# Kernel tuning notes

Measured on AMD Instinct MI355X. Metric: run time of the kernel, lower is better.

Reference implementation:

```python
import jax, jax.numpy as jnp
import numpy as np
from jax import lax

NSAMPLE = 16
NEG_SLOPE = 0.1


def leaky(x):
    return jnp.where(x >= 0, x, NEG_SLOPE * x)


def setup_inputs() -> dict:
    key = jax.random.key(0)
    ks = jax.random.split(key, 8)
    B, N1, N2, D = 4, 4096, 4096, 64
    C_in, C_mid, C_out = D + D + 3, 128, 128  # 131 -> 128 -> 128
    xyz1 = jax.random.normal(ks[0], (B, 3, N1), jnp.float32)
    xyz2 = jax.random.normal(ks[1], (B, 3, N2), jnp.float32)
    points1 = jax.random.normal(ks[2], (B, D, N1), jnp.float32)
    points2 = jax.random.normal(ks[3], (B, D, N2), jnp.float32)
    W1 = jax.random.normal(ks[4], (C_mid, C_in), jnp.float32) * 0.05
    b1 = jnp.zeros((C_mid,), jnp.float32)
    W2 = jax.random.normal(ks[5], (C_out, C_mid), jnp.float32) * 0.05
    b2 = jnp.zeros((C_out,), jnp.float32)
    return {"xyz1": xyz1, "xyz2": xyz2, "points1": points1, "points2": points2,
            "W1": W1, "b1": b1, "W2": W2, "b2": b2}


def reference(xyz1, xyz2, points1, points2, W1, b1, W2, b2):
    B, _, N1 = xyz1.shape
    x1 = jnp.transpose(xyz1, (0, 2, 1))      # [B,N1,3]
    x2 = jnp.transpose(xyz2, (0, 2, 1))      # [B,N2,3]
    p1 = jnp.transpose(points1, (0, 2, 1))   # [B,N1,D1]
    p2 = jnp.transpose(points2, (0, 2, 1))   # [B,N2,D2]

    # knn_point: k smallest squared distances from each x1 point into x2
    d2 = (jnp.sum(x1 * x1, -1)[:, :, None]
          + jnp.sum(x2 * x2, -1)[:, None, :]
          - 2.0 * jnp.einsum('bnc,bmc->bnm', x1, x2))  # [B,N1,N2]
    _, knn_idx = lax.top_k(-d2, NSAMPLE)     # [B,N1,K]

    bidx = jnp.arange(B)[:, None, None]
    neighbor_xyz = x2[bidx, knn_idx]         # [B,N1,K,3]
    direction_xyz = neighbor_xyz - x1[:, :, None, :]
    gp2 = p2[bidx, knn_idx]                  # [B,N1,K,D2]
    gp1 = jnp.broadcast_to(p1[:, :, None, :], (B, N1, NSAMPLE, p1.shape[-1]))
    feat = jnp.concatenate([gp1, gp2, direction_xyz], axis=-1)  # [B,N1,K,131]

    h = leaky(jnp.einsum('oc,bnkc->bnko', W1, feat) + b1)
    h = leaky(jnp.einsum('oc,bnkc->bnko', W2, h) + b2)           # [B,N1,K,C_out]

    dist = jnp.maximum(jnp.linalg.norm(direction_xyz, axis=3), 1e-10)  # [B,N1,K]
    inv = 1.0 / dist
    weights = inv / jnp.sum(inv, axis=2, keepdims=True)          # [B,N1,K]

    cost = jnp.einsum('bnk,bnko->bon', weights, h)               # [B,C_out,N1]
    return cost
```

## Files before the change

### kernel.cpp

```cpp
#include <hip/hip_runtime.h>

typedef unsigned short u16;
typedef unsigned int u32;
typedef unsigned long long u64;
typedef __bf16 bf16x8 __attribute__((ext_vector_type(8)));
typedef float f32x4 __attribute__((ext_vector_type(4)));

#define MFMA16(a, b, c) __builtin_amdgcn_mfma_f32_16x16x32_bf16(a, b, c, 0, 0, 0)

static __device__ __forceinline__ u16 f2bf(float f) {
  union { float f; u32 u; } v; v.f = f;
  u32 u = v.u;
  u32 r = (u + 0x7FFFu + ((u >> 16) & 1u)) >> 16;
  return (u16)r;
}

static __device__ __forceinline__ bf16x8 ld16(const u16* p) {
  return __builtin_bit_cast(bf16x8, *(const uint4*)p);
}

static __device__ __forceinline__ u64 u64min(u64 a, u64 b) { return a < b ? a : b; }

static __device__ __forceinline__ u64 bitonic64(u64 v, int lane) {
#pragma unroll
  for (int k = 2; k <= 64; k <<= 1) {
#pragma unroll
    for (int j = k >> 1; j > 0; j >>= 1) {
      u64 o = __shfl_xor(v, j, 64);
      bool up = ((lane & k) == 0);
      bool lower = ((lane & j) == 0);
      u64 mn = v < o ? v : o;
      u64 mx = v < o ? o : v;
      v = (lower == up) ? mn : mx;
    }
  }
  return v;
}

static __device__ __forceinline__ void bitonic64_2(u64& a, u64& b, int lane) {
#pragma unroll
  for (int k = 2; k <= 64; k <<= 1) {
#pragma unroll
    for (int j = k >> 1; j > 0; j >>= 1) {
      u64 oa = __shfl_xor(a, j, 64);
      u64 ob = __shfl_xor(b, j, 64);
      bool up = ((lane & k) == 0);
      bool lower = ((lane & j) == 0);
      bool sel = (lower == up);
      u64 mna = a < oa ? a : oa, mxa = a < oa ? oa : a;
      u64 mnb = b < ob ? b : ob, mxb = b < ob ? ob : b;
      a = sel ? mna : mxa;
      b = sel ? mnb : mxb;
    }
  }
}

static __device__ __forceinline__ void bitonic32_2(u64& a, u64& b, int lane) {
#pragma unroll
  for (int k = 2; k <= 32; k <<= 1) {
#pragma unroll
    for (int j = k >> 1; j > 0; j >>= 1) {
      u64 oa = __shfl_xor(a, j, 64);
      u64 ob = __shfl_xor(b, j, 64);
      bool up = ((lane & k) == 0);
      bool lower = ((lane & j) == 0);
      bool sel = (lower == up);
      u64 mna = a < oa ? a : oa, mxa = a < oa ? oa : a;
      u64 mnb = b < ob ? b : ob, mxb = b < ob ? ob : b;
      a = sel ? mna : mxa;
      b = sel ? mnb : mxb;
    }
  }
}

static __device__ __forceinline__ u32 fkey(float f) {
  u32 bb = __float_as_uint(f);
  u32 sgn = (u32)((int)bb >> 31);
  return bb ^ (sgn | 0x80000000u);
}

static __device__ __forceinline__ float ikey(u32 k) {
  u32 bb = (k & 0x80000000u) ? (k ^ 0x80000000u) : ~k;
  return __uint_as_float(bb);
}

static __device__ __forceinline__ float d2of(float x, float y, float z, float s1,
                                             f32x4 c) {
  float dt = __builtin_fmaf(z, c[2], __builtin_fmaf(y, c[1], __fmul_rn(x, c[0])));
  return __fsub_rn(__fadd_rn(s1, c[3]), __fmul_rn(2.0f, dt));
}

static __device__ __forceinline__ f32x4 candOf(const float* X2, int m) {
  float cx = X2[m], cy = X2[4096 + m], cz = X2[8192 + m];
  float cs = __fadd_rn(__fadd_rn(__fmul_rn(cx, cx), __fmul_rn(cy, cy)),
                       __fmul_rn(cz, cz));
  f32x4 c = {cx, cy, cz, cs};
  return c;
}

__global__ __launch_bounds__(256, 7) void knn_prep(
    const float* __restrict__ xyz1, const float* __restrict__ xyz2,
    const float* __restrict__ points1, const float* __restrict__ points2,
    const float* __restrict__ W1, const float* __restrict__ W2,
    u16* __restrict__ p1t, u16* __restrict__ p2t,
    u16* __restrict__ W1b, u16* __restrict__ W2b,
    int* __restrict__ knn) {
  __shared__ __align__(16) char LB[8448];
  u16* tile = (u16*)LB;
  u64 (*surv)[2][64] = (u64(*)[2][64])LB;
  const int t = threadIdx.x;
  const int lane = t & 63;
  const int w = t >> 6;
  const int g = blockIdx.x;

  if (g < 144) {
    int i = g * 256 + t;
    if (i < 128 * 160) {
      int r = i / 160, c = i - r * 160;
      W1b[i] = (c < 131) ? f2bf(W1[r * 131 + c]) : (u16)0;
    } else {
      int u = i - 128 * 160;
      W2b[u] = f2bf(W2[u]);
    }
  }

  {
    const bool doT = (g < 512);
    const float* src = (g < 256) ? points1 : points2;
    u16* dst = (g < 256) ? p1t : p2t;
    const int gb = g & 255;
    const int tb = gb >> 6;
    const int n0 = (gb & 63) << 6;
    const float* sp = src + ((size_t)tb << 18);
    if (doT) {
#pragma unroll
      for (int i = 0; i < 16; i++) {
        int d = (i << 2) + (t >> 6);
        int n = t & 63;
        tile[n * 66 + d] = f2bf(sp[((size_t)d << 12) + n0 + n]);
      }
    }
    __syncthreads();
    if (doT) {
      u16* dp = dst + ((size_t)(tb * 4096 + n0) << 6);
#pragma unroll
      for (int i = 0; i < 8; i++) {
        int n = (i << 3) + (t >> 5);
        int dp2 = t & 31;
        *(u32*)(dp + n * 64 + (dp2 << 1)) =
            *(const u32*)(tile + n * 66 + (dp2 << 1));
      }
    }
  }
  __syncthreads();

  const int b = g >> 9;
  const int rbase = (g & 511) << 3;
  const float* X1 = xyz1 + b * 12288;
  const float* X2 = xyz2 + b * 12288;
  {
    const int n0 = rbase + (w << 1);
    const int n1 = n0 + 1;
    const int row0 = b * 4096 + n0;
    const int row1 = row0 + 1;
    const float x0 = X1[n0], y0 = X1[4096 + n0], z0 = X1[8192 + n0];
    const float x1 = X1[n1], y1 = X1[4096 + n1], z1 = X1[8192 + n1];
    const float s10 = __fadd_rn(__fadd_rn(__fmul_rn(x0, x0), __fmul_rn(y0, y0)),
                                __fmul_rn(z0, z0));
    const float s11 = __fadd_rn(__fadd_rn(__fmul_rn(x1, x1), __fmul_rn(y1, y1)),
                                __fmul_rn(z1, z1));

    float fm0 = 3e38f, fm1 = 3e38f;
#pragma unroll 4
    for (int j = 0; j < 64; j++) {
      f32x4 c = candOf(X2, (j << 6) + lane);
      fm0 = fminf(fm0, d2of(x0, y0, z0, s10, c));
      fm1 = fminf(fm1, d2of(x1, y1, z1, s11, c));
    }

    const u32 k0 = fkey(fm0), k1 = fkey(fm1);
    u32 lo0 = 0u, hi0 = 0xFFFFFFFFu, lo1 = 0u, hi1 = 0xFFFFFFFFu;
#pragma unroll
    for (int it = 0; it < 32; it++) {
      u32 md0 = lo0 + ((hi0 - lo0) >> 1);
      u32 md1 = lo1 + ((hi1 - lo1) >> 1);
      bool ge0 = __popcll(__ballot(k0 <= md0)) >= 16;
      bool ge1 = __popcll(__ballot(k1 <= md1)) >= 16;
      hi0 = ge0 ? md0 : hi0;  lo0 = ge0 ? lo0 : md0 + 1;
      hi1 = ge1 ? md1 : hi1;  lo1 = ge1 ? lo1 : md1 + 1;
    }
    const float tau0 = ikey(hi0);
    const float tau1 = ikey(hi1);

    u32 base0 = 0, base1 = 0;
#pragma unroll 4
    for (int j = 0; j < 64; j++) {
      const int m = (j << 6) + lane;
      f32x4 c = candOf(X2, m);
      float d0 = d2of(x0, y0, z0, s10, c);
      float d1 = d2of(x1, y1, z1, s11, c);
      bool p0 = d0 <= tau0;
      bool p1 = d1 <= tau1;
      u64 mk0 = __ballot(p0);
      u64 mk1 = __ballot(p1);
      if (mk0) {
        if (p0) {
          u32 pre = __builtin_amdgcn_mbcnt_lo((u32)mk0, 0u);
          pre = __builtin_amdgcn_mbcnt_hi((u32)(mk0 >> 32), pre);
          u32 slot = base0 + pre;
          if (slot < 64u) surv[w][0][slot] = ((u64)fkey(d0) << 32) | (u32)m;
        }
        base0 += (u32)__popcll(mk0);
      }
      if (mk1) {
        if (p1) {
          u32 pre = __builtin_amdgcn_mbcnt_lo((u32)mk1, 0u);
          pre = __builtin_amdgcn_mbcnt_hi((u32)(mk1 >> 32), pre);
          u32 slot = base1 + pre;
          if (slot < 64u) surv[w][1][slot] = ((u64)fkey(d1) << 32) | (u32)m;
        }
        base1 += (u32)__popcll(mk1);
      }
    }
    const u32 S0 = base0, S1 = base1;

    const u32 Smax = max(S0, S1);
    if (Smax <= 32) {
      u64 v0 = (lane < (int)S0) ? surv[w][0][lane] : ~0ull;
      u64 v1 = (lane < (int)S1) ? surv[w][1][lane] : ~0ull;
      bitonic32_2(v0, v1, lane);
      if (lane < 16) {
        knn[row0 * 16 + lane] = (int)(v0 & 0xFFFFFFFFull);
        knn[row1 * 16 + lane] = (int)(v1 & 0xFFFFFFFFull);
      }
    } else if (Smax <= 64) {
      u64 v0 = (lane < (int)S0) ? surv[w][0][lane] : ~0ull;
      u64 v1 = (lane < (int)S1) ? surv[w][1][lane] : ~0ull;
      bitonic64_2(v0, v1, lane);
      if (lane < 16) {
        knn[row0 * 16 + lane] = (int)(v0 & 0xFFFFFFFFull);
        knn[row1 * 16 + lane] = (int)(v1 & 0xFFFFFFFFull);
      }
    } else {
#pragma unroll 1
      for (int p = 0; p < 2; p++) {
        const u32 S = p ? S1 : S0;
        const int row = p ? row1 : row0;
        const float xx = p ? x1 : x0, yy = p ? y1 : y0, zz = p ? z1 : z0;
        const float ss = p ? s11 : s10;
        if (S <= 64) {
          u64 v = (lane < (int)S) ? surv[w][p][lane] : ~0ull;
          v = bitonic64(v, lane);
          if (lane < 16) knn[row * 16 + lane] = (int)(v & 0xFFFFFFFFull);
        } else {
          u64 prev = 0;
          for (int rr = 0; rr < 16; rr++) {
            u64 lm = ~0ull;
#pragma unroll 4
            for (int j = 0; j < 64; j++) {
              const int m = (j << 6) + lane;
              f32x4 c = candOf(X2, m);
              float d = d2of(xx, yy, zz, ss, c);
              u64 k64 = ((u64)fkey(d) << 32) | (u32)m;
              if (k64 > prev && k64 < lm) lm = k64;
            }
            u64 gm = lm;
#pragma unroll
            for (int off = 32; off; off >>= 1)
              gm = u64min(gm, __shfl_xor(gm, off, 64));
            if (lane == 0) knn[row * 16 + rr] = (int)(gm & 0xFFFFFFFFull);
            prev = gm;
          }
        }
      }
    }
  }
}

__global__ __launch_bounds__(256, 3) void mlp_kernel(
    const float* __restrict__ xyz1, const float* __restrict__ xyz2,
    const u16* __restrict__ p1t, const u16* __restrict__ p2t,
    const int* __restrict__ knn,
    const u16* __restrict__ W1b, const float* __restrict__ b1,
    const u16* __restrict__ W2b, const float* __restrict__ b2,
    float* __restrict__ out) {
  __shared__ __align__(16) u16 F[128 * 168];
  __shared__ __align__(16) float winv[128];
  __shared__ __align__(16) float wnorm[128];
  __shared__ __align__(16) float outbuf[128 * 12];
  const int t = threadIdx.x;
  const int g = blockIdx.x;
  const int b = g >> 9;
  const int rbase = (g & 511) << 3;

  {
    const int m = t >> 1, half = t & 1;
    const int n1 = rbase + (m >> 4);
    const uint4* s1p = (const uint4*)(p1t + ((size_t)(b * 4096 + n1) << 6)) + half * 4;
    uint4* d1p = (uint4*)(F + m * 168) + half * 4;
    d1p[0] = s1p[0]; d1p[1] = s1p[1]; d1p[2] = s1p[2]; d1p[3] = s1p[3];
    const int idx = knn[(((size_t)(b * 4096 + n1)) << 4) + (m & 15)];
    const uint4* s2p = (const uint4*)(p2t + ((size_t)(b * 4096 + idx) << 6)) + half * 4;
    uint4* d2p = (uint4*)(F + m * 168 + 64) + half * 4;
    d2p[0] = s2p[0]; d2p[1] = s2p[1]; d2p[2] = s2p[2]; d2p[3] = s2p[3];
  }
  if (t < 128) {
    const int m = t;
    const int n1 = rbase + (m >> 4);
    const int idx = knn[(((size_t)(b * 4096 + n1)) << 4) + (m & 15)];
    const float* X1 = xyz1 + b * 12288;
    const float* X2 = xyz2 + b * 12288;
    float dx = X2[idx] - X1[n1];
    float dy = X2[4096 + idx] - X1[4096 + n1];
    float dz = X2[8192 + idx] - X1[8192 + n1];
    u32 u0 = (u32)f2bf(dx) | ((u32)f2bf(dy) << 16);
    u32 u1 = (u32)f2bf(dz);
    uint4 pk = make_uint4(u0, u1, 0u, 0u);
    *(uint4*)(F + m * 168 + 128) = pk;
    float d = sqrtf(dx * dx + dy * dy + dz * dz);
    winv[m] = 1.0f / fmaxf(d, 1e-10f);
  } else {
    const int m = t - 128;
    uint4 zz = make_uint4(0u, 0u, 0u, 0u);
    uint4* zp = (uint4*)(F + m * 168 + 136);
    zp[0] = zz; zp[1] = zz; zp[2] = zz; zp[3] = zz;
  }
  __syncthreads();

  if (t < 128) {
    const int r = t >> 4;
    float s = 0.f;
#pragma unroll
    for (int k = 0; k < 16; k++) s += winv[(r << 4) + k];
    wnorm[t] = winv[t] / s;
  }

  const int lane = t & 63;
  const int wid = t >> 6;
  const int l15 = lane & 15;
  const int quad = lane >> 4;
  const int koff = quad << 3;
  const int nbase = wid << 5;

  f32x4 acc[8][2];
  const f32x4 z4 = {0.f, 0.f, 0.f, 0.f};
#pragma unroll
  for (int i = 0; i < 8; i++)
#pragma unroll
    for (int j = 0; j < 2; j++) acc[i][j] = z4;

#pragma unroll
  for (int s = 0; s < 5; s++) {
    bf16x8 bf0 = ld16(W1b + (nbase + l15) * 160 + s * 32 + koff);
    bf16x8 bf1 = ld16(W1b + (nbase + 16 + l15) * 160 + s * 32 + koff);
#pragma unroll
    for (int mt = 0; mt < 8; mt++) {
      bf16x8 a = ld16(F + (mt * 16 + l15) * 168 + s * 32 + koff);
      acc[mt][0] = MFMA16(a, bf0, acc[mt][0]);
      acc[mt][1] = MFMA16(a, bf1, acc[mt][1]);
    }
  }
  __syncthreads();

  {
    const float bv0 = b1[nbase + l15];
    const float bv1 = b1[nbase + 16 + l15];
#pragma unroll
    for (int mt = 0; mt < 8; mt++) {
      u16* hrow = F + (mt * 16 + quad * 4) * 168;
#pragma unroll
      for (int r = 0; r < 4; r++) {
        float zv0 = acc[mt][0][r] + bv0;
        zv0 = (zv0 >= 0.f) ? zv0 : 0.1f * zv0;
        hrow[r * 168 + nbase + l15] = f2bf(zv0);
        float zv1 = acc[mt][1][r] + bv1;
        zv1 = (zv1 >= 0.f) ? zv1 : 0.1f * zv1;
        hrow[r * 168 + nbase + 16 + l15] = f2bf(zv1);
      }
    }
  }
  __syncthreads();

  f32x4 acc2[8][2];
#pragma unroll
  for (int i = 0; i < 8; i++)
#pragma unroll
    for (int j = 0; j < 2; j++) acc2[i][j] = z4;

#pragma unroll
  for (int s = 0; s < 4; s++) {
    bf16x8 bf0 = ld16(W2b + (nbase + l15) * 128 + s * 32 + koff);
    bf16x8 bf1 = ld16(W2b + (nbase + 16 + l15) * 128 + s * 32 + koff);
#pragma unroll
    for (int mt = 0; mt < 8; mt++) {
      bf16x8 a = ld16(F + (mt * 16 + l15) * 168 + s * 32 + koff);
      acc2[mt][0] = MFMA16(a, bf0, acc2[mt][0]);
      acc2[mt][1] = MFMA16(a, bf1, acc2[mt][1]);
    }
  }

  {
    const float bv0 = b2[nbase + l15];
    const float bv1 = b2[nbase + 16 + l15];
#pragma unroll
    for (int mt = 0; mt < 8; mt++) {
      const f32x4 w4 = *(const f32x4*)&wnorm[(mt << 4) + (quad << 2)];
      float p0 = 0.f, p1 = 0.f;
#pragma unroll
      for (int r = 0; r < 4; r++) {
        float zv0 = acc2[mt][0][r] + bv0;
        zv0 = (zv0 >= 0.f) ? zv0 : 0.1f * zv0;
        p0 += zv0 * w4[r];
        float zv1 = acc2[mt][1][r] + bv1;
        zv1 = (zv1 >= 0.f) ? zv1 : 0.1f * zv1;
        p1 += zv1 * w4[r];
      }
      p0 += __shfl_xor(p0, 16); p0 += __shfl_xor(p0, 32);
      p1 += __shfl_xor(p1, 16); p1 += __shfl_xor(p1, 32);
      if (quad == 0) {
        outbuf[(nbase + l15) * 12 + mt] = p0;
        outbuf[(nbase + 16 + l15) * 12 + mt] = p1;
      }
    }
  }
  __syncthreads();
  {
    const int ch = t >> 1, half = t & 1;
    f32x4 v = *(const f32x4*)&outbuf[ch * 12 + (half << 2)];
    float* op = out + (((size_t)(b * 128 + ch)) << 12) + rbase + (half << 2);
    *(f32x4*)op = v;
  }
}

extern "C" void kernel_launch(void* const* d_in, const int* in_sizes, int n_in,
                              void* d_out, int out_size, void* d_ws, size_t ws_size,
                              hipStream_t stream) {
  const float* xyz1 = (const float*)d_in[0];
  const float* xyz2 = (const float*)d_in[1];
  const float* points1 = (const float*)d_in[2];
  const float* points2 = (const float*)d_in[3];
  const float* W1 = (const float*)d_in[4];
  const float* b1 = (const float*)d_in[5];
  const float* W2 = (const float*)d_in[6];
  const float* b2 = (const float*)d_in[7];
  float* out = (float*)d_out;

  char* ws = (char*)d_ws;
  int* knn = (int*)ws;
  u16* p1t = (u16*)(ws + 1048576);
  u16* p2t = (u16*)(ws + 3145728);
  u16* W1b = (u16*)(ws + 5242880);
  u16* W2b = (u16*)(ws + 5283840);

  hipLaunchKernelGGL(knn_prep, dim3(2048), dim3(256), 0, stream,
                     xyz1, xyz2, points1, points2, W1, W2, p1t, p2t, W1b, W2b, knn);
  hipLaunchKernelGGL(mlp_kernel, dim3(2048), dim3(256), 0, stream,
                     xyz1, xyz2, p1t, p2t, knn, W1b, b1, W2b, b2, out);
}
```

Baseline: 149.2 us.

## Stage candidate xyz and norms in LDS, use packed distance math

The kNN kernel now runs 512-thread blocks, each handling 16 query rows. Each block stages half of the candidate points, as xyz plus squared norm, into 32KB of LDS at a time. All 8 waves then read the precomputed candidates from LDS instead of reloading from global memory and recomputing norms per wave. Distances for the two query rows are computed with 2-wide vector FMAs, and the threshold bisection drops from 32 to 24 iterations. The trade-offs are extra block-wide barriers, a larger LDS footprint that lowers occupancy, slight rounding changes from the fused multiply-add, and a looser threshold that can admit more survivors.

```diff
diff --git a/kernel.cpp b/kernel.cpp
--- a/kernel.cpp
+++ b/kernel.cpp
@@ -5,6 +5,7 @@
 typedef unsigned long long u64;
 typedef __bf16 bf16x8 __attribute__((ext_vector_type(8)));
 typedef float f32x4 __attribute__((ext_vector_type(4)));
+typedef float f32x2 __attribute__((ext_vector_type(2)));
 
 #define MFMA16(a, b, c) __builtin_amdgcn_mfma_f32_16x16x32_bf16(a, b, c, 0, 0, 0)
 
@@ -90,6 +91,18 @@
   return __fsub_rn(__fadd_rn(s1, c[3]), __fmul_rn(2.0f, dt));
 }
 
+static __device__ __forceinline__ f32x2 d2of2(f32x2 X, f32x2 Y, f32x2 Z,
+                                              f32x2 S, f32x4 c) {
+  f32x2 cx = {c[0], c[0]}, cy = {c[1], c[1]}, cz = {c[2], c[2]},
+        cs = {c[3], c[3]};
+  f32x2 m = X * cx;
+  f32x2 t = __builtin_elementwise_fma(Y, cy, m);
+  f32x2 dt = __builtin_elementwise_fma(Z, cz, t);
+  f32x2 sa = S + cs;
+  const f32x2 n2 = {-2.0f, -2.0f};
+  return __builtin_elementwise_fma(dt, n2, sa);
+}
+
 static __device__ __forceinline__ f32x4 candOf(const float* X2, int m) {
   float cx = X2[m], cy = X2[4096 + m], cz = X2[8192 + m];
   float cs = __fadd_rn(__fadd_rn(__fmul_rn(cx, cx), __fmul_rn(cy, cy)),
@@ -98,23 +111,24 @@
   return c;
 }
 
-__global__ __launch_bounds__(256, 7) void knn_prep(
+__global__ __launch_bounds__(512, 4) void knn_prep(
     const float* __restrict__ xyz1, const float* __restrict__ xyz2,
     const float* __restrict__ points1, const float* __restrict__ points2,
     const float* __restrict__ W1, const float* __restrict__ W2,
     u16* __restrict__ p1t, u16* __restrict__ p2t,
     u16* __restrict__ W1b, u16* __restrict__ W2b,
     int* __restrict__ knn) {
-  __shared__ __align__(16) char LB[8448];
+  __shared__ __align__(16) char LB[32768];
+  f32x4* candL = (f32x4*)LB;
   u16* tile = (u16*)LB;
-  u64 (*surv)[2][64] = (u64(*)[2][64])LB;
+  __shared__ u64 surv[8][2][64];
   const int t = threadIdx.x;
   const int lane = t & 63;
   const int w = t >> 6;
   const int g = blockIdx.x;
 
-  if (g < 144) {
-    int i = g * 256 + t;
+  if (g < 72) {
+    int i = g * 512 + t;
     if (i < 128 * 160) {
       int r = i / 160, c = i - r * 160;
       W1b[i] = (c < 131) ? f2bf(W1[r * 131 + c]) : (u16)0;
@@ -134,8 +148,8 @@
     const float* sp = src + ((size_t)tb << 18);
     if (doT) {
 #pragma unroll
-      for (int i = 0; i < 16; i++) {
-        int d = (i << 2) + (t >> 6);
+      for (int i = 0; i < 8; i++) {
+        int d = (i << 3) + (t >> 6);
         int n = t & 63;
         tile[n * 66 + d] = f2bf(sp[((size_t)d << 12) + n0 + n]);
       }
@@ -144,18 +158,17 @@
     if (doT) {
       u16* dp = dst + ((size_t)(tb * 4096 + n0) << 6);
 #pragma unroll
-      for (int i = 0; i < 8; i++) {
-        int n = (i << 3) + (t >> 5);
+      for (int i = 0; i < 4; i++) {
+        int n = (i << 4) + (t >> 5);
         int dp2 = t & 31;
         *(u32*)(dp + n * 64 + (dp2 << 1)) =
             *(const u32*)(tile + n * 66 + (dp2 << 1));
       }
     }
   }
-  __syncthreads();
-
-  const int b = g >> 9;
-  const int rbase = (g & 511) << 3;
+
+  const int b = g >> 8;
+  const int rbase = (g & 255) << 4;
   const float* X1 = xyz1 + b * 12288;
   const float* X2 = xyz2 + b * 12288;
   {
@@ -169,19 +182,41 @@
                                 __fmul_rn(z0, z0));
     const float s11 = __fadd_rn(__fadd_rn(__fmul_rn(x1, x1), __fmul_rn(y1, y1)),
                                 __fmul_rn(z1, z1));
+    const f32x2 X01 = {x0, x1}, Y01 = {y0, y1}, Z01 = {z0, z1},
+                S01 = {s10, s11};
+
+    auto STAGE = [&](int h) {
+      __syncthreads();
+#pragma unroll
+      for (int i = 0; i < 4; i++) {
+        int ml = (i << 9) + t;
+        int m = (h << 11) + ml;
+        float x = X2[m], y = X2[4096 + m], z = X2[8192 + m];
+        float s2 = __fadd_rn(__fadd_rn(__fmul_rn(x, x), __fmul_rn(y, y)),
+                             __fmul_rn(z, z));
+        f32x4 pk = {x, y, z, s2};
+        candL[ml] = pk;
+      }
+      __syncthreads();
+    };
 
     float fm0 = 3e38f, fm1 = 3e38f;
-#pragma unroll 4
-    for (int j = 0; j < 64; j++) {
-      f32x4 c = candOf(X2, (j << 6) + lane);
-      fm0 = fminf(fm0, d2of(x0, y0, z0, s10, c));
-      fm1 = fminf(fm1, d2of(x1, y1, z1, s11, c));
+#pragma unroll 1
+    for (int h = 0; h < 2; h++) {
+      STAGE(h);
+#pragma unroll 8
+      for (int jl = 0; jl < 32; jl++) {
+        f32x4 c = candL[(jl << 6) + lane];
+        f32x2 d01 = d2of2(X01, Y01, Z01, S01, c);
+        fm0 = fminf(fm0, d01[0]);
+        fm1 = fminf(fm1, d01[1]);
+      }
     }
 
     const u32 k0 = fkey(fm0), k1 = fkey(fm1);
     u32 lo0 = 0u, hi0 = 0xFFFFFFFFu, lo1 = 0u, hi1 = 0xFFFFFFFFu;
 #pragma unroll
-    for (int it = 0; it < 32; it++) {
+    for (int it = 0; it < 24; it++) {
       u32 md0 = lo0 + ((hi0 - lo0) >> 1);
       u32 md1 = lo1 + ((hi1 - lo1) >> 1);
       bool ge0 = __popcll(__ballot(k0 <= md0)) >= 16;
@@ -193,33 +228,37 @@
     const float tau1 = ikey(hi1);
 
     u32 base0 = 0, base1 = 0;
+#pragma unroll 1
+    for (int h = 0; h < 2; h++) {
+      STAGE(h);
 #pragma unroll 4
-    for (int j = 0; j < 64; j++) {
-      const int m = (j << 6) + lane;
-      f32x4 c = candOf(X2, m);
-      float d0 = d2of(x0, y0, z0, s10, c);
-      float d1 = d2of(x1, y1, z1, s11, c);
-      bool p0 = d0 <= tau0;
-      bool p1 = d1 <= tau1;
-      u64 mk0 = __ballot(p0);
-      u64 mk1 = __ballot(p1);
-      if (mk0) {
-        if (p0) {
-          u32 pre = __builtin_amdgcn_mbcnt_lo((u32)mk0, 0u);
-          pre = __builtin_amdgcn_mbcnt_hi((u32)(mk0 >> 32), pre);
-          u32 slot = base0 + pre;
-          if (slot < 64u) surv[w][0][slot] = ((u64)fkey(d0) << 32) | (u32)m;
+      for (int jl = 0; jl < 32; jl++) {
+        const int m = (h << 11) + (jl << 6) + lane;
+        f32x4 c = candL[(jl << 6) + lane];
+        f32x2 d01 = d2of2(X01, Y01, Z01, S01, c);
+        float d0 = d01[0], d1 = d01[1];
+        bool p0 = d0 <= tau0;
+        bool p1 = d1 <= tau1;
+        u64 mk0 = __ballot(p0);
+        u64 mk1 = __ballot(p1);
+        if (mk0) {
+          if (p0) {
+            u32 pre = __builtin_amdgcn_mbcnt_lo((u32)mk0, 0u);
+            pre = __builtin_amdgcn_mbcnt_hi((u32)(mk0 >> 32), pre);
+            u32 slot = base0 + pre;
+            if (slot < 64u) surv[w][0][slot] = ((u64)fkey(d0) << 32) | (u32)m;
+          }
+          base0 += (u32)__popcll(mk0);
         }
-        base0 += (u32)__popcll(mk0);
-      }
-      if (mk1) {
-        if (p1) {
-          u32 pre = __builtin_amdgcn_mbcnt_lo((u32)mk1, 0u);
-          pre = __builtin_amdgcn_mbcnt_hi((u32)(mk1 >> 32), pre);
-          u32 slot = base1 + pre;
-          if (slot < 64u) surv[w][1][slot] = ((u64)fkey(d1) << 32) | (u32)m;
+        if (mk1) {
+          if (p1) {
+            u32 pre = __builtin_amdgcn_mbcnt_lo((u32)mk1, 0u);
+            pre = __builtin_amdgcn_mbcnt_hi((u32)(mk1 >> 32), pre);
+            u32 slot = base1 + pre;
+            if (slot < 64u) surv[w][1][slot] = ((u64)fkey(d1) << 32) | (u32)m;
+          }
+          base1 += (u32)__popcll(mk1);
         }
-        base1 += (u32)__popcll(mk1);
       }
     }
     const u32 S0 = base0, S1 = base1;
@@ -452,7 +491,7 @@
   u16* W1b = (u16*)(ws + 5242880);
   u16* W2b = (u16*)(ws + 5283840);
 
-  hipLaunchKernelGGL(knn_prep, dim3(2048), dim3(256), 0, stream,
+  hipLaunchKernelGGL(knn_prep, dim3(1024), dim3(512), 0, stream,
                      xyz1, xyz2, points1, points2, W1, W2, p1t, p2t, W1b, W2b, knn);
   hipLaunchKernelGGL(mlp_kernel, dim3(2048), dim3(256), 0, stream,
                      xyz1, xyz2, p1t, p2t, knn, W1b, b1, W2b, b2, out);
```

Result: faster. 143.7 us (-3.7%).
